# Performance work log

Hardware: AMD Instinct MI355X
Metric: run time of the kernel (lower is better)

The kernel has to match this reference:

```python
import jax, jax.numpy as jnp
import numpy as np
import math

ANSWER_LEN = 11; D_MODEL = 6; FFN_DIM = 3; HEAD_DIM = 3; MAX_SEQ_LEN = 34
N_HEADS = 2; POS_DIM = 3; TOK_DIM = 3; VOCAB_SIZE = 14; MAX_DIGITS = 10
EOS_TOKEN = 12; EQUALS_TOKEN = 11; PAD_TOKEN = 13; PLUS_TOKEN = 10
B, T = 65536, 34


def _spiral(i, period):
    return (math.cos(2 * math.pi * i / period), math.sin(2 * math.pi * i / period), i / max(period - 1, 1))


def _build_pos_enc():
    N_POS = 10
    pe = np.zeros((MAX_SEQ_LEN, POS_DIM), dtype=np.float32)
    for i in range(MAX_DIGITS):
        pe[i] = _spiral(i, N_POS)
    for i in range(MAX_DIGITS):
        pe[11 + i] = _spiral(i, N_POS)
    for i in range(min(ANSWER_LEN, N_POS)):
        pe[22 + i] = _spiral(i, N_POS)
    pe[32] = [0.0, 0.0, 1.5]
    pe[10] = [2.0, 0.0, -1.0]
    pe[21] = [0.0, 2.0, -1.0]
    pe[33] = [-2.0, 0.0, -1.0]
    return pe


def _build_tok_emb():
    emb = np.zeros((VOCAB_SIZE, TOK_DIM), dtype=np.float32)
    for d in range(10):
        emb[d] = _spiral(d, 10)
    emb[PLUS_TOKEN] = [2.0, 0.0, -1.0]
    emb[EQUALS_TOKEN] = [0.0, 2.0, -1.0]
    emb[EOS_TOKEN] = [-2.0, 0.0, -1.0]
    emb[PAD_TOKEN] = [0.0, -2.0, -1.0]
    return emb


def setup_inputs() -> dict:
    key = jax.random.key(0)
    ks = jax.random.split(key, 12)
    H = N_HEADS * HEAD_DIM  # 6

    def lin(k, out_d, in_d):
        bound = 1.0 / math.sqrt(in_d)
        return jax.random.uniform(k, (out_d, in_d), jnp.float32, -bound, bound)

    return {
        'idx': jax.random.randint(ks[0], (B, T), 0, VOCAB_SIZE),
        'tok_emb': jnp.asarray(_build_tok_emb()),
        'pos_enc': jnp.asarray(_build_pos_enc()),
        'q_w': lin(ks[1], H, POS_DIM),
        'k_w': lin(ks[2], H, POS_DIM),
        'v_w': lin(ks[3], H, TOK_DIM),
        'out_w': lin(ks[4], D_MODEL, H),
        'ln1_g': jnp.ones((D_MODEL,)), 'ln1_b': jnp.zeros((D_MODEL,)),
        'ln2_g': jnp.ones((D_MODEL,)), 'ln2_b': jnp.zeros((D_MODEL,)),
        'lnf_g': jnp.ones((D_MODEL,)), 'lnf_b': jnp.zeros((D_MODEL,)),
        'ffn_w1': lin(ks[5], FFN_DIM, D_MODEL),
        'ffn_b1': jax.random.uniform(ks[6], (FFN_DIM,), jnp.float32, -1/math.sqrt(D_MODEL), 1/math.sqrt(D_MODEL)),
        'ffn_w2': lin(ks[7], D_MODEL, FFN_DIM),
        'ffn_b2': jax.random.uniform(ks[8], (D_MODEL,), jnp.float32, -1/math.sqrt(FFN_DIM), 1/math.sqrt(FFN_DIM)),
        'head_w': lin(ks[9], TOK_DIM, D_MODEL),
    }


def _ln(x, g, b, eps=1e-5):
    mu = jnp.mean(x, -1, keepdims=True)
    var = jnp.mean((x - mu) ** 2, -1, keepdims=True)
    return (x - mu) * jax.lax.rsqrt(var + eps) * g + b


def reference(idx, tok_emb, pos_enc, q_w, k_w, v_w, out_w,
              ln1_g, ln1_b, ln2_g, ln2_b, lnf_g, lnf_b,
              ffn_w1, ffn_b1, ffn_w2, ffn_b2, head_w):
    b, t = idx.shape
    tok = tok_emb[idx]                              # [B,T,3]
    pos = jnp.broadcast_to(pos_enc[:t][None], (b, t, POS_DIM))
    x = jnp.concatenate([tok, pos], -1)             # [B,T,6]
    h = _ln(x, ln1_g, ln1_b)
    x_tok, x_pos = h[..., :TOK_DIM], h[..., TOK_DIM:]
    q = (x_pos @ q_w.T).reshape(b, t, N_HEADS, HEAD_DIM)
    k = (x_pos @ k_w.T).reshape(b, t, N_HEADS, HEAD_DIM)
    v = (x_tok @ v_w.T).reshape(b, t, N_HEADS, HEAD_DIM)
    attn = jnp.einsum('bqhd,bkhd->bhqk', q, k) / math.sqrt(HEAD_DIM)
    mask = jnp.tril(jnp.ones((t, t), dtype=bool))
    attn = jnp.where(mask[None, None], attn, -jnp.inf)
    attn = jax.nn.softmax(attn, -1)
    out = jnp.einsum('bhqk,bkhd->bqhd', attn, v).reshape(b, t, N_HEADS * HEAD_DIM)
    x = x + out @ out_w.T
    h2 = _ln(x, ln2_g, ln2_b)
    ffn = jax.nn.gelu(h2 @ ffn_w1.T + ffn_b1, approximate=False) @ ffn_w2.T + ffn_b2
    x = x + ffn
    x = _ln(x, lnf_g, lnf_b)
    return (x @ head_w.T) @ tok_emb.T               # [B,T,VOCAB]
```

## Files before the change

kernel.cpp:

```cpp
#include <hip/hip_runtime.h>
#include <math.h>

#define TT  34
#define VV  14
#define BLK 256
#define NPB 512

typedef float v2f __attribute__((ext_vector_type(2)));
typedef float v4f __attribute__((ext_vector_type(4)));

#if __has_builtin(__builtin_amdgcn_exp2f)
#define EXP2F(x) __builtin_amdgcn_exp2f(x)
#else
#define EXP2F(x) exp2f(x)
#endif
#if __has_builtin(__builtin_amdgcn_rcpf)
#define RCPF(x) __builtin_amdgcn_rcpf(x)
#else
#define RCPF(x) (1.0f/(x))
#endif

static __device__ __forceinline__ v2f fma2(v2f a, v2f b, v2f c) {
    return __builtin_elementwise_fma(a, b, c);
}
static __device__ __forceinline__ v2f bc2(float s) { v2f r; r.x = s; r.y = s; return r; }
#define SV2(v, a, b) __builtin_shufflevector((v), (v), (a), (b))
#define LD2(i) (*reinterpret_cast<const v2f*>(&wsm[(i)]))


static __device__ __forceinline__ void epi_store(
    const float* __restrict__ wsm, const float o6[6], const float x[6],
    float* __restrict__ outp, int elem1)
{
    v2f X0 = {x[0], x[1]}, X1 = {x[2], x[3]}, X2 = {x[4], x[5]};
    #pragma unroll
    for (int j = 0; j < 6; ++j) {
        const v2f oj = bc2(o6[j]);
        X0 = fma2(oj, LD2(j * 6 + 0), X0);
        X1 = fma2(oj, LD2(j * 6 + 2), X1);
        X2 = fma2(oj, LD2(j * 6 + 4), X2);
    }
    {
        v2f S = X0 + X1 + X2;
        const float mu = (S.x + S.y) * (1.0f / 6.0f);
        const v2f muv = bc2(mu);
        const v2f D0 = X0 - muv, D1 = X1 - muv, D2 = X2 - muv;
        v2f E = fma2(D0, D0, fma2(D1, D1, D2 * D2));
        const float rstd = rsqrtf((E.x + E.y) * (1.0f / 6.0f) + 1e-5f);
        const v2f rs = bc2(rstd);
        const v2f H0 = fma2(D0 * rs, LD2(36), LD2(42));
        const v2f H1 = fma2(D1 * rs, LD2(38), LD2(44));
        const v2f H2 = fma2(D2 * rs, LD2(40), LD2(46));
        const float h[6] = {H0.x, H0.y, H1.x, H1.y, H2.x, H2.y};
        v2f F = LD2(66);
        float f2 = wsm[68];
        #pragma unroll
        for (int d = 0; d < 6; ++d) {
            F  = fma2(bc2(h[d]), LD2(48 + 2 * d), F);
            f2 = fmaf(h[d], wsm[60 + d], f2);
        }
        float g3[3];
        g3[0] = 0.5f * F.x * (1.0f + erff(F.x * 0.70710678118654752f));
        g3[1] = 0.5f * F.y * (1.0f + erff(F.y * 0.70710678118654752f));
        g3[2] = 0.5f * f2  * (1.0f + erff(f2  * 0.70710678118654752f));
        X0 += LD2(88); X1 += LD2(90); X2 += LD2(92);
        #pragma unroll
        for (int i = 0; i < 3; ++i) {
            const v2f gi = bc2(g3[i]);
            X0 = fma2(gi, LD2(70 + i * 6 + 0), X0);
            X1 = fma2(gi, LD2(70 + i * 6 + 2), X1);
            X2 = fma2(gi, LD2(70 + i * 6 + 4), X2);
        }
    }
    v2f lgv[7];
    {
        v2f S = X0 + X1 + X2;
        const float mu = (S.x + S.y) * (1.0f / 6.0f);
        const v2f muv = bc2(mu);
        const v2f D0 = X0 - muv, D1 = X1 - muv, D2 = X2 - muv;
        v2f E = fma2(D0, D0, fma2(D1, D1, D2 * D2));
        const float rstd = rsqrtf((E.x + E.y) * (1.0f / 6.0f) + 1e-5f);
        const float xd[6] = {D0.x, D0.y, D1.x, D1.y, D2.x, D2.y};
        v2f D01 = {0.f, 0.f};
        float d2 = 0.f;
        #pragma unroll
        for (int d = 0; d < 6; ++d) {
            D01 = fma2(bc2(xd[d]), LD2(96 + 2 * d), D01);
            d2  = fmaf(xd[d], wsm[108 + d], d2);
        }
        const v2f y01 = fma2(bc2(rstd), D01, LD2(118));
        const float y2 = fmaf(rstd, d2, wsm[120]);
        const v2f Y0 = bc2(y01.x), Y1 = bc2(y01.y), Y2 = bc2(y2);
        #pragma unroll
        for (int mm = 0; mm < 7; ++mm)
            lgv[mm] = fma2(Y0, LD2(122 + 2 * mm),
                      fma2(Y1, LD2(136 + 2 * mm),
                           Y2 * LD2(150 + 2 * mm)));
    }
    if (!elem1) {
        v4f w0; w0.x = lgv[0].x; w0.y = lgv[0].y; w0.z = lgv[1].x; w0.w = lgv[1].y;
        v4f w1; w1.x = lgv[2].x; w1.y = lgv[2].y; w1.z = lgv[3].x; w1.w = lgv[3].y;
        v4f w2; w2.x = lgv[4].x; w2.y = lgv[4].y; w2.z = lgv[5].x; w2.w = lgv[5].y;
        *reinterpret_cast<v4f*>(outp + 0) = w0;
        *reinterpret_cast<v4f*>(outp + 4) = w1;
        *reinterpret_cast<v4f*>(outp + 8) = w2;
        *reinterpret_cast<v2f*>(outp + 12) = lgv[6];
    } else {
        *reinterpret_cast<v2f*>(outp + 0) = lgv[0];
        v4f w0; w0.x = lgv[1].x; w0.y = lgv[1].y; w0.z = lgv[2].x; w0.w = lgv[2].y;
        v4f w1; w1.x = lgv[3].x; w1.y = lgv[3].y; w1.z = lgv[4].x; w1.w = lgv[4].y;
        v4f w2; w2.x = lgv[5].x; w2.y = lgv[5].y; w2.z = lgv[6].x; w2.w = lgv[6].y;
        *reinterpret_cast<v4f*>(outp + 2)  = w0;
        *reinterpret_cast<v4f*>(outp + 6)  = w1;
        *reinterpret_cast<v4f*>(outp + 10) = w2;
    }
}

static __device__ __forceinline__ void make_q(
    const float* __restrict__ ln1_g, const float* __restrict__ ln1_b,
    const float* __restrict__ q_w, const float x[6],
    v2f& Q03, v2f& Q14, v2f& Q25)
{
    float mu = (x[0] + x[1] + x[2] + x[3] + x[4] + x[5]) * (1.0f / 6.0f);
    float var = 0.0f;
    #pragma unroll
    for (int d = 0; d < 6; ++d) { float dd = x[d] - mu; var += dd * dd; }
    const float rstd = rsqrtf(var * (1.0f / 6.0f) + 1e-5f);
    const float h3 = (x[3] - mu) * rstd * ln1_g[3] + ln1_b[3];
    const float h4 = (x[4] - mu) * rstd * ln1_g[4] + ln1_b[4];
    const float h5 = (x[5] - mu) * rstd * ln1_g[5] + ln1_b[5];
    float q[6];
    #pragma unroll
    for (int r = 0; r < 6; ++r)
        q[r] = h3 * q_w[r * 3 + 0] + h4 * q_w[r * 3 + 1] + h5 * q_w[r * 3 + 2];
    Q03.x = q[0]; Q03.y = q[3];
    Q14.x = q[1]; Q14.y = q[4];
    Q25.x = q[2]; Q25.y = q[5];
}

__global__ __launch_bounds__(BLK) void addtx_fwd(
    const int*   __restrict__ idx,
    const float* __restrict__ tok_emb,
    const float* __restrict__ pos_enc,
    const float* __restrict__ q_w,
    const float* __restrict__ k_w,
    const float* __restrict__ v_w,
    const float* __restrict__ out_w,
    const float* __restrict__ ln1_g, const float* __restrict__ ln1_b,
    const float* __restrict__ ln2_g, const float* __restrict__ ln2_b,
    const float* __restrict__ lnf_g, const float* __restrict__ lnf_b,
    const float* __restrict__ ffn_w1, const float* __restrict__ ffn_b1,
    const float* __restrict__ ffn_w2, const float* __restrict__ ffn_b2,
    const float* __restrict__ head_w,
    float* __restrict__ out, int n)
{
    __shared__ v4f   kvs[TT * VV * 3];
    __shared__ float wsm[308];
    __shared__ int   idsb[17 * TT];

    const int tid = threadIdx.x;
    const int blk = blockIdx.x;

    for (int i = tid; i < 308; i += BLK) {
        float val = 0.0f;
        if (i < 36)       { const int j = i / 6, d = i - j * 6; val = out_w[d * 6 + j]; }
        else if (i < 42)  val = ln2_g[i - 36];
        else if (i < 48)  val = ln2_b[i - 42];
        else if (i < 60)  { const int k = i - 48, d = k >> 1, ii = k & 1; val = ffn_w1[ii * 6 + d]; }
        else if (i < 66)  val = ffn_w1[12 + (i - 60)];
        else if (i < 69)  val = ffn_b1[i - 66];
        else if (i < 70)  val = 0.0f;
        else if (i < 88)  { const int k = i - 70, ii = k / 6, d = k - ii * 6; val = ffn_w2[d * 3 + ii]; }
        else if (i < 94)  val = ffn_b2[i - 88];
        else if (i < 96)  val = 0.0f;
        else if (i < 108) { const int k = i - 96, d = k >> 1, c = k & 1; val = lnf_g[d] * head_w[c * 6 + d]; }
        else if (i < 114) { const int d = i - 108; val = lnf_g[d] * head_w[12 + d]; }
        else if (i < 118) val = 0.0f;
        else if (i < 121) { const int c = i - 118; float s = 0.0f;
                            #pragma unroll
                            for (int d = 0; d < 6; ++d) s += lnf_b[d] * head_w[c * 6 + d];
                            val = s; }
        else if (i < 122) val = 0.0f;
        else if (i < 164) { const int k = i - 122, c = k / 14, v = k - c * 14; val = tok_emb[v * 3 + c]; }
        else if (i < 206) val = tok_emb[i - 164];
        else              val = pos_enc[i - 206];
        wsm[i] = val;
    }

    const int p0 = blk * BLK;
    const int b0 = p0 / 17;
    {
        const int gb = b0 * TT;
        for (int e = tid; e < 17 * TT; e += BLK) {
            const int g = gb + e;
            idsb[e] = (g < n) ? (idx[g] * 48) : 0;
        }
    }

    const float rs3l = 0.57735026918962576f * 1.4426950408889634f;
    for (int e = tid; e < TT * VV; e += BLK) {
        const int pos = e / VV, id = e - pos * VV;
        float x[6];
        x[0] = tok_emb[id * 3 + 0]; x[1] = tok_emb[id * 3 + 1]; x[2] = tok_emb[id * 3 + 2];
        x[3] = pos_enc[pos * 3 + 0]; x[4] = pos_enc[pos * 3 + 1]; x[5] = pos_enc[pos * 3 + 2];
        float mu = (x[0] + x[1] + x[2] + x[3] + x[4] + x[5]) * (1.0f / 6.0f);
        float var = 0.0f;
        #pragma unroll
        for (int d = 0; d < 6; ++d) { float dd = x[d] - mu; var += dd * dd; }
        const float rstd = rsqrtf(var * (1.0f / 6.0f) + 1e-5f);
        float h[6];
        #pragma unroll
        for (int d = 0; d < 6; ++d) h[d] = (x[d] - mu) * rstd * ln1_g[d] + ln1_b[d];
        float kk[6], vvv[6];
        #pragma unroll
        for (int r = 0; r < 6; ++r) {
            kk[r]  = (h[3] * k_w[r * 3 + 0] + h[4] * k_w[r * 3 + 1] + h[5] * k_w[r * 3 + 2]) * rs3l;
            vvv[r] =  h[0] * v_w[r * 3 + 0] + h[1] * v_w[r * 3 + 1] + h[2] * v_w[r * 3 + 2];
        }
        v4f f0; f0.x = kk[0]; f0.y = kk[3]; f0.z = kk[1]; f0.w = kk[4];
        v4f f1; f1.x = kk[2]; f1.y = kk[5]; f1.z = vvv[0]; f1.w = vvv[3];
        v4f f2; f2.x = vvv[1]; f2.y = vvv[4]; f2.z = vvv[2]; f2.w = vvv[5];
        kvs[e * 3 + 0] = f0;
        kvs[e * 3 + 1] = f1;
        kvs[e * 3 + 2] = f2;
    }
    __syncthreads();

    const int srank = (tid + ((blk & 3) << 6)) & (BLK - 1);
    const int r0 = p0 % 17;
    const int thrA = 15 * r0;
    int u, k;
    if (srank < thrA)           { u = srank / 15;      k = srank - 15 * u; }
    else if (srank < thrA + 16) { u = r0;              k = srank - thrA;   }
    else                        { const int rr = srank - 1; u = rr / 15; k = rr - 15 * u; }
    int dd17 = u - r0; if (dd17 < 0) dd17 += 17;
    const int pl = dd17 + 17 * k;
    const int p  = p0 + pl;
    const int b  = p / 17;
    const int t0 = 2 * (p - b * 17);
    const int t1 = t0 + 1;
    const int* __restrict__ rowL = idsb + (b - b0) * TT;

    float xa[6], xb[6];
    {
        const int ta3 = rowL[t0] >> 4;
        const int tb3 = rowL[t1] >> 4;
        xa[0] = wsm[164 + ta3]; xa[1] = wsm[165 + ta3]; xa[2] = wsm[166 + ta3];
        xb[0] = wsm[164 + tb3]; xb[1] = wsm[165 + tb3]; xb[2] = wsm[166 + tb3];
        xa[3] = wsm[206 + t0 * 3]; xa[4] = wsm[207 + t0 * 3]; xa[5] = wsm[208 + t0 * 3];
        xb[3] = wsm[206 + t1 * 3]; xb[4] = wsm[207 + t1 * 3]; xb[5] = wsm[208 + t1 * 3];
    }
    v2f Q03a, Q14a, Q25a, Q03b, Q14b, Q25b;
    make_q(ln1_g, ln1_b, q_w, xa, Q03a, Q14a, Q25a);
    make_q(ln1_g, ln1_b, q_w, xb, Q03b, Q14b, Q25b);

    v2f La = {0.f, 0.f}, A0a = {0.f, 0.f}, A1a = {0.f, 0.f}, A2a = {0.f, 0.f};
    v2f Lb = {0.f, 0.f}, A0b = {0.f, 0.f}, A1b = {0.f, 0.f}, A2b = {0.f, 0.f};
    int ids48 = rowL[0];
    const char* kp = (const char*)kvs;
    for (int s = 0; s <= t0; ++s) {
        const v4f* e4 = (const v4f*)(kp + ids48);
        const v4f ka = e4[0], kb = e4[1], vb = e4[2];
        ids48 = rowL[s + 1];
        const v2f ka01 = SV2(ka, 0, 1), ka23 = SV2(ka, 2, 3);
        const v2f kb01 = SV2(kb, 0, 1), kb23 = SV2(kb, 2, 3);
        const v2f vb01 = SV2(vb, 0, 1), vb23 = SV2(vb, 2, 3);
        v2f sa = fma2(Q03a, ka01, fma2(Q14a, ka23, Q25a * kb01));
        v2f sb = fma2(Q03b, ka01, fma2(Q14b, ka23, Q25b * kb01));
        v2f pa; pa.x = EXP2F(sa.x); pa.y = EXP2F(sa.y);
        v2f pb; pb.x = EXP2F(sb.x); pb.y = EXP2F(sb.y);
        La += pa; Lb += pb;
        A0a = fma2(pa, kb23, A0a); A0b = fma2(pb, kb23, A0b);
        A1a = fma2(pa, vb01, A1a); A1b = fma2(pb, vb01, A1b);
        A2a = fma2(pa, vb23, A2a); A2b = fma2(pb, vb23, A2b);
        kp += VV * 48;
    }
    {
        const v4f* e4 = (const v4f*)(kp + ids48);
        const v4f ka = e4[0], kb = e4[1], vb = e4[2];
        v2f sb = fma2(Q03b, SV2(ka, 0, 1),
                 fma2(Q14b, SV2(ka, 2, 3), Q25b * SV2(kb, 0, 1)));
        v2f pb; pb.x = EXP2F(sb.x); pb.y = EXP2F(sb.y);
        Lb += pb;
        A0b = fma2(pb, SV2(kb, 2, 3), A0b);
        A1b = fma2(pb, SV2(vb, 0, 1), A1b);
        A2b = fma2(pb, SV2(vb, 2, 3), A2b);
    }

    v2f Ia; Ia.x = RCPF(La.x); Ia.y = RCPF(La.y);
    v2f Ib; Ib.x = RCPF(Lb.x); Ib.y = RCPF(Lb.y);
    const v2f Oa0 = A0a * Ia, Oa1 = A1a * Ia, Oa2 = A2a * Ia;
    const v2f Ob0 = A0b * Ib, Ob1 = A1b * Ib, Ob2 = A2b * Ib;
    const float o6a[6] = {Oa0.x, Oa1.x, Oa2.x, Oa0.y, Oa1.y, Oa2.y};
    const float o6b[6] = {Ob0.x, Ob1.x, Ob2.x, Ob0.y, Ob1.y, Ob2.y};

    float* __restrict__ outp = out + (size_t)(b * TT + t0) * VV;
    epi_store(wsm, o6a, xa, outp,      0);
    epi_store(wsm, o6b, xb, outp + VV, 1);
}

extern "C" void kernel_launch(void* const* d_in, const int* in_sizes, int n_in,
                              void* d_out, int out_size, void* d_ws, size_t ws_size,
                              hipStream_t stream) {
    const int*   idx     = (const int*)  d_in[0];
    const float* tok_emb = (const float*)d_in[1];
    const float* pos_enc = (const float*)d_in[2];
    const float* q_w     = (const float*)d_in[3];
    const float* k_w     = (const float*)d_in[4];
    const float* v_w     = (const float*)d_in[5];
    const float* out_w   = (const float*)d_in[6];
    const float* ln1_g   = (const float*)d_in[7];
    const float* ln1_b   = (const float*)d_in[8];
    const float* ln2_g   = (const float*)d_in[9];
    const float* ln2_b   = (const float*)d_in[10];
    const float* lnf_g   = (const float*)d_in[11];
    const float* lnf_b   = (const float*)d_in[12];
    const float* ffn_w1  = (const float*)d_in[13];
    const float* ffn_b1  = (const float*)d_in[14];
    const float* ffn_w2  = (const float*)d_in[15];
    const float* ffn_b2  = (const float*)d_in[16];
    const float* head_w  = (const float*)d_in[17];
    float* out = (float*)d_out;

    const int n = in_sizes[0];
    const int blocks = n / NPB;
    addtx_fwd<<<blocks, BLK, 0, stream>>>(idx, tok_emb, pos_enc, q_w, k_w, v_w, out_w,
                                          ln1_g, ln1_b, ln2_g, ln2_b, lnf_g, lnf_b,
                                          ffn_w1, ffn_b1, ffn_w2, ffn_b2, head_w, out, n);
}
```

Baseline: 218.6 us.

## Double block size to amortize shared-table setup and recompute inputs to cut registers

Block size goes from 256 to 512 threads, with a launch-bounds occupancy hint. The K/V table built per block in shared memory is now shared by twice as many positions, halving how often it is rebuilt. The row-to-thread work assignment is rewritten for the new block size. The per-position inputs are no longer kept alive across the attention loop; they are reloaded from shared memory in the query and epilogue steps to lower register pressure. The cost is an extra shared-memory read and larger blocks that may schedule less flexibly.

```diff
diff --git a/kernel.cpp b/kernel.cpp
--- a/kernel.cpp
+++ b/kernel.cpp
@@ -3,8 +3,7 @@
 
 #define TT  34
 #define VV  14
-#define BLK 256
-#define NPB 512
+#define BLK 512
 
 typedef float v2f __attribute__((ext_vector_type(2)));
 typedef float v4f __attribute__((ext_vector_type(4)));
@@ -29,10 +28,13 @@
 
 
 static __device__ __forceinline__ void epi_store(
-    const float* __restrict__ wsm, const float o6[6], const float x[6],
+    const float* __restrict__ wsm, const float o6[6], int tb3, int t,
     float* __restrict__ outp, int elem1)
 {
-    v2f X0 = {x[0], x[1]}, X1 = {x[2], x[3]}, X2 = {x[4], x[5]};
+    v2f X0, X1, X2;
+    X0.x = wsm[164 + tb3];   X0.y = wsm[165 + tb3];
+    X1.x = wsm[166 + tb3];   X1.y = wsm[206 + t * 3];
+    X2.x = wsm[207 + t * 3]; X2.y = wsm[208 + t * 3];
     #pragma unroll
     for (int j = 0; j < 6; ++j) {
         const v2f oj = bc2(o6[j]);
@@ -117,10 +119,14 @@
 }
 
 static __device__ __forceinline__ void make_q(
+    const float* __restrict__ wsm,
     const float* __restrict__ ln1_g, const float* __restrict__ ln1_b,
-    const float* __restrict__ q_w, const float x[6],
+    const float* __restrict__ q_w, int tb3, int t,
     v2f& Q03, v2f& Q14, v2f& Q25)
 {
+    float x[6];
+    x[0] = wsm[164 + tb3];   x[1] = wsm[165 + tb3]; x[2] = wsm[166 + tb3];
+    x[3] = wsm[206 + t * 3]; x[4] = wsm[207 + t * 3]; x[5] = wsm[208 + t * 3];
     float mu = (x[0] + x[1] + x[2] + x[3] + x[4] + x[5]) * (1.0f / 6.0f);
     float var = 0.0f;
     #pragma unroll
@@ -138,7 +144,7 @@
     Q25.x = q[2]; Q25.y = q[5];
 }
 
-__global__ __launch_bounds__(BLK) void addtx_fwd(
+__global__ __launch_bounds__(BLK, 8) void addtx_fwd(
     const int*   __restrict__ idx,
     const float* __restrict__ tok_emb,
     const float* __restrict__ pos_enc,
@@ -156,12 +162,13 @@
 {
     __shared__ v4f   kvs[TT * VV * 3];
     __shared__ float wsm[308];
-    __shared__ int   idsb[17 * TT];
+    __shared__ int   idsb[1088];
 
     const int tid = threadIdx.x;
     const int blk = blockIdx.x;
 
-    for (int i = tid; i < 308; i += BLK) {
+    if (tid < 308) {
+        const int i = tid;
         float val = 0.0f;
         if (i < 36)       { const int j = i / 6, d = i - j * 6; val = out_w[d * 6 + j]; }
         else if (i < 42)  val = ln2_g[i - 36];
@@ -191,7 +198,7 @@
     const int b0 = p0 / 17;
     {
         const int gb = b0 * TT;
-        for (int e = tid; e < 17 * TT; e += BLK) {
+        for (int e = tid; e < 1088; e += BLK) {
             const int g = gb + e;
             idsb[e] = (g < n) ? (idx[g] * 48) : 0;
         }
@@ -226,33 +233,31 @@
     }
     __syncthreads();
 
-    const int srank = (tid + ((blk & 3) << 6)) & (BLK - 1);
-    const int r0 = p0 % 17;
-    const int thrA = 15 * r0;
+    const int srank = (tid + ((blk & 7) << 6)) & (BLK - 1);
+    const int r0p = p0 % 17;
     int u, k;
-    if (srank < thrA)           { u = srank / 15;      k = srank - 15 * u; }
-    else if (srank < thrA + 16) { u = r0;              k = srank - thrA;   }
-    else                        { const int rr = srank - 1; u = rr / 15; k = rr - 15 * u; }
-    int dd17 = u - r0; if (dd17 < 0) dd17 += 17;
-    const int pl = dd17 + 17 * k;
+    if (r0p <= 15) {
+        const int thrA = 30 * r0p;
+        if (srank < thrA)           { u = srank / 30;              k = srank - 30 * u; }
+        else if (srank < thrA + 62) { const int rr = srank - thrA; u = r0p + rr / 31;  k = rr % 31; }
+        else                        { const int rr = srank - thrA - 62;
+                                      const int qq = rr / 30;      u = r0p + 2 + qq;   k = rr - 30 * qq; }
+    } else {
+        if (srank < 31)        { u = 0;                      k = srank; }
+        else if (srank < 481)  { const int rr = srank - 31;  u = 1 + rr / 30; k = rr % 30; }
+        else                   { u = 16;                     k = srank - 481; }
+    }
+    int dlt = u - r0p; if (dlt < 0) dlt += 17;
+    const int pl = dlt + 17 * k;
     const int p  = p0 + pl;
     const int b  = p / 17;
     const int t0 = 2 * (p - b * 17);
     const int t1 = t0 + 1;
     const int* __restrict__ rowL = idsb + (b - b0) * TT;
 
-    float xa[6], xb[6];
-    {
-        const int ta3 = rowL[t0] >> 4;
-        const int tb3 = rowL[t1] >> 4;
-        xa[0] = wsm[164 + ta3]; xa[1] = wsm[165 + ta3]; xa[2] = wsm[166 + ta3];
-        xb[0] = wsm[164 + tb3]; xb[1] = wsm[165 + tb3]; xb[2] = wsm[166 + tb3];
-        xa[3] = wsm[206 + t0 * 3]; xa[4] = wsm[207 + t0 * 3]; xa[5] = wsm[208 + t0 * 3];
-        xb[3] = wsm[206 + t1 * 3]; xb[4] = wsm[207 + t1 * 3]; xb[5] = wsm[208 + t1 * 3];
-    }
     v2f Q03a, Q14a, Q25a, Q03b, Q14b, Q25b;
-    make_q(ln1_g, ln1_b, q_w, xa, Q03a, Q14a, Q25a);
-    make_q(ln1_g, ln1_b, q_w, xb, Q03b, Q14b, Q25b);
+    make_q(wsm, ln1_g, ln1_b, q_w, rowL[t0] >> 4, t0, Q03a, Q14a, Q25a);
+    make_q(wsm, ln1_g, ln1_b, q_w, rowL[t1] >> 4, t1, Q03b, Q14b, Q25b);
 
     v2f La = {0.f, 0.f}, A0a = {0.f, 0.f}, A1a = {0.f, 0.f}, A2a = {0.f, 0.f};
     v2f Lb = {0.f, 0.f}, A0b = {0.f, 0.f}, A1b = {0.f, 0.f}, A2b = {0.f, 0.f};
@@ -287,16 +292,19 @@
         A2b = fma2(pb, SV2(vb, 2, 3), A2b);
     }
 
-    v2f Ia; Ia.x = RCPF(La.x); Ia.y = RCPF(La.y);
-    v2f Ib; Ib.x = RCPF(Lb.x); Ib.y = RCPF(Lb.y);
-    const v2f Oa0 = A0a * Ia, Oa1 = A1a * Ia, Oa2 = A2a * Ia;
-    const v2f Ob0 = A0b * Ib, Ob1 = A1b * Ib, Ob2 = A2b * Ib;
-    const float o6a[6] = {Oa0.x, Oa1.x, Oa2.x, Oa0.y, Oa1.y, Oa2.y};
-    const float o6b[6] = {Ob0.x, Ob1.x, Ob2.x, Ob0.y, Ob1.y, Ob2.y};
-
     float* __restrict__ outp = out + (size_t)(b * TT + t0) * VV;
-    epi_store(wsm, o6a, xa, outp,      0);
-    epi_store(wsm, o6b, xb, outp + VV, 1);
+    {
+        v2f Ia; Ia.x = RCPF(La.x); Ia.y = RCPF(La.y);
+        const v2f O0 = A0a * Ia, O1 = A1a * Ia, O2 = A2a * Ia;
+        const float o6a[6] = {O0.x, O1.x, O2.x, O0.y, O1.y, O2.y};
+        epi_store(wsm, o6a, rowL[t0] >> 4, t0, outp, 0);
+    }
+    {
+        v2f Ib; Ib.x = RCPF(Lb.x); Ib.y = RCPF(Lb.y);
+        const v2f O0 = A0b * Ib, O1 = A1b * Ib, O2 = A2b * Ib;
+        const float o6b[6] = {O0.x, O1.x, O2.x, O0.y, O1.y, O2.y};
+        epi_store(wsm, o6b, rowL[t1] >> 4, t1, outp + VV, 1);
+    }
 }
 
 extern "C" void kernel_launch(void* const* d_in, const int* in_sizes, int n_in,
@@ -323,7 +331,7 @@
     float* out = (float*)d_out;
 
     const int n = in_sizes[0];
-    const int blocks = n / NPB;
+    const int blocks = n / (2 * BLK);
     addtx_fwd<<<blocks, BLK, 0, stream>>>(idx, tok_emb, pos_enc, q_w, k_w, v_w, out_w,
                                           ln1_g, ln1_b, ln2_g, ln2_b, lnf_g, lnf_b,
                                           ffn_w1, ffn_b1, ffn_w2, ffn_b2, head_w, out, n);
```

Measured after the change: 393.6 us. 80.1% more time.
